# Kernel tuning notes

Hardware: AMD Instinct MI355X
Metric: run time of the kernel (lower is better)

The kernel has to match this reference:

```python
import jax, jax.numpy as jnp
import numpy as np

B, C, L = 16, 256, 2048

def setup_inputs() -> dict:
    key = jax.random.key(0)
    k1, k2, k3, k4 = jax.random.split(key, 4)
    return {
        "proj_query": jax.random.normal(k1, (B, C, L), dtype=jnp.float32),
        "proj_key": jax.random.normal(k2, (B, C, L), dtype=jnp.float32),
        "proj_val": jax.random.normal(k3, (B, C, L), dtype=jnp.float32),
        "padding_mask": jax.random.uniform(k4, (B, 1, L), dtype=jnp.float32),
    }

def reference(proj_query, proj_key, proj_val, padding_mask):
    c = proj_query.shape[1]
    # energy[b,l,m] = sum_c Q[b,c,l] * K[b,c,m]  -> (B, L, L)
    energy = jnp.einsum("bcl,bcm->blm", proj_query, proj_key) / jnp.sqrt(jnp.float32(c))
    # log-additive padding mask (the tril mask in the source is dead code, never applied)
    logits = energy + jnp.log(padding_mask + 1e-9)
    attention = jax.nn.softmax(logits, axis=-1)
    # post-softmax multiplicative mask
    attention = attention * padding_mask
    # out[b,c,l] = sum_m V[b,c,m] * attention[b,l,m]  -> (B, C, L)
    out = jnp.einsum("bcm,blm->bcl", proj_val, attention)
    return out
```

## Files before the change

kernel.cpp:

```cpp
#include <hip/hip_runtime.h>
#include <hip/hip_bf16.h>

#define B_ 16
#define C_ 256
#define L_ 2048
#define MT 32

typedef __attribute__((ext_vector_type(8))) short bf16x8;
typedef __attribute__((ext_vector_type(4))) float f32x4;

#define CEXP 0.09016844005556021f

__device__ __forceinline__ short f2bf_rne(float f) {
    union { float f; unsigned u; } x; x.f = f;
    unsigned r = x.u + 0x7fffu + ((x.u >> 16) & 1u);
    return (short)(r >> 16);
}

__device__ __forceinline__ void gld_lds16(const void* g, void* l) {
    __builtin_amdgcn_global_load_lds(
        (const __attribute__((address_space(1))) void*)g,
        (__attribute__((address_space(3))) void*)l, 16, 0, 0);
}

__global__ __launch_bounds__(256) void prepass_kernel(
        const float* __restrict__ Kin, const float* __restrict__ Vin,
        const float* __restrict__ mask,
        short* __restrict__ Kt, short* __restrict__ Vb) {
    const int bid = blockIdx.x;
    const int t = threadIdx.x;
    if (bid < 512) {
        __shared__ unsigned short tile[64 * 256];
        const int b  = bid >> 5;
        const int l0 = (bid & 31) * 64;
        #pragma unroll
        for (int iter = 0; iter < 16; ++iter) {
            int idx = iter * 256 + t;
            int ci = idx >> 4;
            int lc = (idx & 15) * 4;
            float4 v = *(const float4*)(Kin + ((size_t)(b * C_ + ci)) * L_ + l0 + lc);
            float vv[4] = {v.x, v.y, v.z, v.w};
            #pragma unroll
            for (int j = 0; j < 4; ++j) {
                int l = lc + j;
                tile[l * 256 + (((ci >> 3) ^ (l & 31)) << 3) + (ci & 7)] =
                    (unsigned short)f2bf_rne(vv[j]);
            }
        }
        __syncthreads();
        #pragma unroll
        for (int iter = 0; iter < 8; ++iter) {
            int li = iter * 8 + (t >> 5);
            int ck = t & 31;
            uint4 val = *(const uint4*)(tile + li * 256 + ((ck ^ (li & 31)) << 3));
            *(uint4*)(Kt + ((size_t)(b * L_ + l0 + li)) * C_ + ck * 8) = val;
        }
    } else {
        size_t e = ((size_t)(bid - 512) * 256 + t) * 8;
        int b = (int)(e >> 19);
        int m = (int)(e & (L_ - 1));
        const float4 v0 = *(const float4*)(Vin + e);
        const float4 v1 = *(const float4*)(Vin + e + 4);
        const float* mp = mask + ((size_t)b << 11) + m;
        const float4 m0 = *(const float4*)mp;
        const float4 m1 = *(const float4*)(mp + 4);
        uint4 o;
        o.x = (unsigned)(unsigned short)f2bf_rne(v0.x * m0.x)
            | ((unsigned)(unsigned short)f2bf_rne(v0.y * m0.y) << 16);
        o.y = (unsigned)(unsigned short)f2bf_rne(v0.z * m0.z)
            | ((unsigned)(unsigned short)f2bf_rne(v0.w * m0.w) << 16);
        o.z = (unsigned)(unsigned short)f2bf_rne(v1.x * m1.x)
            | ((unsigned)(unsigned short)f2bf_rne(v1.y * m1.y) << 16);
        o.w = (unsigned)(unsigned short)f2bf_rne(v1.z * m1.z)
            | ((unsigned)(unsigned short)f2bf_rne(v1.w * m1.w) << 16);
        *(uint4*)(Vb + e) = o;
    }
}

__device__ __forceinline__ void stage_K(const short* __restrict__ Ksrc,
                                        short* Ks, int m0, int t) {
    #pragma unroll
    for (int rr = 0; rr < 2; ++rr) {
        int G = rr * 512 + t;
        int m = G >> 5, p = G & 31;
        gld_lds16(Ksrc + ((size_t)(m0 + m) << 8) + ((p ^ m) << 3), Ks + G * 8);
    }
}

__device__ __forceinline__ void load_V(bf16x8 (&vf)[2], const short* __restrict__ Vw, int m0) {
    #pragma unroll
    for (int ct = 0; ct < 2; ++ct)
        vf[ct] = *(const bf16x8*)(Vw + (size_t)(ct * 16) * L_ + m0);
}

#define O_PHASE(PBUF, VF)                                                                  \
  {                                                                                        \
    _Pragma("unroll")                                                                      \
    for (int lt = 0; lt < 4; ++lt) {                                                       \
      bf16x8 af = *(const bf16x8*)((PBUF) + (16 * lt + 4 * (n & 3) + (n >> 2)) * 40 + 8 * q); \
      _Pragma("unroll")                                                                    \
      for (int ct = 0; ct < 2; ++ct)                                                       \
        Oacc[lt][ct] =                                                                     \
            __builtin_amdgcn_mfma_f32_16x16x32_bf16(af, (VF)[ct], Oacc[lt][ct], 0, 0, 0);  \
    }                                                                                      \
  }

#define S_PHASE(KS, PW0)                                                                   \
  {                                                                                        \
    f32x4 Sa = fzero, Sb = fzero;                                                          \
    const short* Krow = (KS) + (16 * mt + n) * 256;                                        \
    _Pragma("unroll")                                                                      \
    for (int ks = 0; ks < 4; ++ks) {                                                       \
      bf16x8 bfa = *(const bf16x8*)(Krow + (((4 * ks + q) ^ (16 * mt + n)) << 3));         \
      bf16x8 bfb = *(const bf16x8*)(Krow + (((4 * (ks + 4) + q) ^ (16 * mt + n)) << 3));   \
      Sa = __builtin_amdgcn_mfma_f32_16x16x32_bf16(qf[ks], bfa, Sa, 0, 0, 0);              \
      Sb = __builtin_amdgcn_mfma_f32_16x16x32_bf16(qf[ks + 4], bfb, Sb, 0, 0, 0);          \
    }                                                                                      \
    _Pragma("unroll")                                                                      \
    for (int r = 0; r < 4; ++r) {                                                          \
      float p0 = wv * exp2f(Sa[r] + Sb[r]);                                                \
      dn[r] += p0;                                                                         \
      (PW0)[(4 * r) * 40] = f2bf_rne(p0);                                                  \
    }                                                                                      \
  }

__global__ __launch_bounds__(512, 4) void attn_main(
        const float* __restrict__ Qin,
        const short* __restrict__ Kt,
        const short* __restrict__ Vb,
        const float* __restrict__ mask,
        float* __restrict__ out) {
    __shared__ __align__(16) char smem[43520];
    short* KsB0 = (short*)smem;
    short* KsB1 = (short*)(smem + 16384);
    short* PA   = (short*)(smem + 32768);
    short* PB   = (short*)(smem + 37888);
    float* Dsh  = (float*)(smem + 43008);

    const int t = threadIdx.x;
    const int w = t >> 6, lane = t & 63, q = lane >> 4, n = lane & 15;
    const int g = w & 3, mt = w >> 2;

    const int b  = blockIdx.x & 15;
    const int l0 = (blockIdx.x >> 4) * 64;

    const short* Ksrc = Kt + (size_t)b * (L_ * C_);
    const short* Vsrc = Vb + (size_t)b * (C_ * L_);
    const float* mrow = mask + (size_t)b * L_;
    const short* Vw   = Vsrc + (size_t)(32 * w + n) * L_ + 8 * q;
    short* Pw0A = PA + (16 * g + q) * 40 + 16 * mt + n;
    short* Pw0B = PB + (16 * g + q) * 40 + 16 * mt + n;

    bf16x8 qf[8];
    {
        const float* Qb = Qin + (size_t)b * (C_ * L_) + (l0 + 16 * g + n);
        #pragma unroll
        for (int ks = 0; ks < 8; ++ks) {
            bf16x8 v;
            #pragma unroll
            for (int j = 0; j < 8; ++j) {
                float f = Qb[(size_t)(32 * ks + 8 * q + j) * L_];
                v[j] = f2bf_rne(f * CEXP);
            }
            qf[ks] = v;
        }
    }

    const f32x4 fzero = {0.f, 0.f, 0.f, 0.f};
    f32x4 Oacc[4][2];
    #pragma unroll
    for (int i = 0; i < 4; ++i)
        #pragma unroll
        for (int j = 0; j < 2; ++j) Oacc[i][j] = fzero;
    float dn[4] = {0.f, 0.f, 0.f, 0.f};

    stage_K(Ksrc, KsB0, 0, t);
    bf16x8 vfA[2], vfB[2];
    load_V(vfA, Vw, 0);
    float wv = mrow[16 * mt + n] + 1e-9f;

    #pragma unroll 1
    for (int it2 = 0; it2 < L_ / MT / 2; ++it2) {
        const int m0a = it2 * (2 * MT);
        const int m0b = m0a + MT;

        __syncthreads();
        if (m0a != 0) O_PHASE(PB, vfB)
        stage_K(Ksrc, KsB1, m0a + MT, t);
        load_V(vfB, Vw, m0a + MT);
        float wvn0 = mrow[m0a + MT + 16 * mt + n] + 1e-9f;
        S_PHASE(KsB0, Pw0A)
        wv = wvn0;

        __syncthreads();
        O_PHASE(PA, vfA)
        float wvn1 = 0.f;
        if (m0b + MT < L_) {
            stage_K(Ksrc, KsB0, m0b + MT, t);
            load_V(vfA, Vw, m0b + MT);
            wvn1 = mrow[m0b + MT + 16 * mt + n] + 1e-9f;
        }
        S_PHASE(KsB1, Pw0B)
        wv = wvn1;
    }

    __syncthreads();
    O_PHASE(PB, vfB)

    #pragma unroll
    for (int d = 1; d < 16; d <<= 1) {
        #pragma unroll
        for (int r = 0; r < 4; ++r)
            dn[r] += __shfl_xor(dn[r], d, 64);
    }
    if (n == 0) {
        #pragma unroll
        for (int r = 0; r < 4; ++r)
            Dsh[mt * 64 + 16 * g + 4 * q + r] = dn[r];
    }
    __syncthreads();

    float rden[4][4];
    #pragma unroll
    for (int lt = 0; lt < 4; ++lt)
        #pragma unroll
        for (int r = 0; r < 4; ++r) {
            int l = 16 * lt + 4 * q + r;
            rden[lt][r] = 1.0f / (Dsh[l] + Dsh[64 + l]);
        }

    float* ob = out + (size_t)b * (C_ * L_) + l0;
    #pragma unroll
    for (int lt = 0; lt < 4; ++lt)
        #pragma unroll
        for (int ct = 0; ct < 2; ++ct) {
            int c = 32 * w + 16 * ct + n;
            float4 val;
            val.x = Oacc[lt][ct][0] * rden[lt][0];
            val.y = Oacc[lt][ct][1] * rden[lt][1];
            val.z = Oacc[lt][ct][2] * rden[lt][2];
            val.w = Oacc[lt][ct][3] * rden[lt][3];
            *(float4*)(ob + (size_t)c * L_ + 16 * lt + 4 * q) = val;
        }
}

extern "C" void kernel_launch(void* const* d_in, const int* in_sizes, int n_in,
                              void* d_out, int out_size, void* d_ws, size_t ws_size,
                              hipStream_t stream) {
    const float* Q    = (const float*)d_in[0];
    const float* K    = (const float*)d_in[1];
    const float* V    = (const float*)d_in[2];
    const float* mask = (const float*)d_in[3];
    float* out = (float*)d_out;

    short* Kt = (short*)d_ws;
    short* Vb = Kt + (size_t)B_ * L_ * C_;

    prepass_kernel<<<4608, 256, 0, stream>>>(K, V, mask, Kt, Vb);
    attn_main<<<512, 512, 0, stream>>>(Q, Kt, Vb, mask, out);
}
```

Measured before the change: 236.7 us.

## Restructure attention into per-wave 32x32 MFMA tiles with register-resident P

Replaces the 16x16x32 MFMA split, where waves shared S/P through LDS buffers, with a layout in which each wave owns 32 query rows across all 256 channels. It uses 32x32x16 MFMAs and keeps the probability tile in registers, feeding it straight into the PV MFMA. This removes the LDS round-trip and cross-wave dependency for P and reads V directly from global memory. The launch changes to 256 blocks of 256 threads at one block per CU. That raises register pressure and lowers occupancy, which risks poor latency hiding of the global V loads.

Measured after the change: 413.3 us. +74.6%, slower.

```diff
diff --git a/kernel.cpp b/kernel.cpp
--- a/kernel.cpp
+++ b/kernel.cpp
@@ -4,10 +4,13 @@
 #define B_ 16
 #define C_ 256
 #define L_ 2048
-#define MT 32
+#define KVB 32
+#define NT (L_ / KVB)
 
 typedef __attribute__((ext_vector_type(8))) short bf16x8;
-typedef __attribute__((ext_vector_type(4))) float f32x4;
+typedef __attribute__((ext_vector_type(4))) short bf16x4;
+typedef __attribute__((ext_vector_type(4))) unsigned u32x4;
+typedef __attribute__((ext_vector_type(16))) float f32x16;
 
 #define CEXP 0.09016844005556021f
 
@@ -80,167 +83,146 @@
 __device__ __forceinline__ void stage_K(const short* __restrict__ Ksrc,
                                         short* Ks, int m0, int t) {
     #pragma unroll
-    for (int rr = 0; rr < 2; ++rr) {
-        int G = rr * 512 + t;
+    for (int rr = 0; rr < 4; ++rr) {
+        int G = rr * 256 + t;
         int m = G >> 5, p = G & 31;
         gld_lds16(Ksrc + ((size_t)(m0 + m) << 8) + ((p ^ m) << 3), Ks + G * 8);
     }
 }
 
-__device__ __forceinline__ void load_V(bf16x8 (&vf)[2], const short* __restrict__ Vw, int m0) {
-    #pragma unroll
-    for (int ct = 0; ct < 2; ++ct)
-        vf[ct] = *(const bf16x8*)(Vw + (size_t)(ct * 16) * L_ + m0);
-}
-
-#define O_PHASE(PBUF, VF)                                                                  \
-  {                                                                                        \
-    _Pragma("unroll")                                                                      \
-    for (int lt = 0; lt < 4; ++lt) {                                                       \
-      bf16x8 af = *(const bf16x8*)((PBUF) + (16 * lt + 4 * (n & 3) + (n >> 2)) * 40 + 8 * q); \
-      _Pragma("unroll")                                                                    \
-      for (int ct = 0; ct < 2; ++ct)                                                       \
-        Oacc[lt][ct] =                                                                     \
-            __builtin_amdgcn_mfma_f32_16x16x32_bf16(af, (VF)[ct], Oacc[lt][ct], 0, 0, 0);  \
-    }                                                                                      \
+#define TILE_BODY(KS, M0)                                                                   \
+  {                                                                                         \
+    const short* Krow = (KS) + ln * 256;                                                    \
+    bf16x8 kf[16];                                                                          \
+    _Pragma("unroll")                                                                       \
+    for (int ki = 0; ki < 16; ++ki)                                                         \
+      kf[ki] = *(const bf16x8*)(Krow + (((2 * ki + h) ^ ln) << 3));                         \
+    bf16x4 vq[8][4];                                                                        \
+    _Pragma("unroll")                                                                       \
+    for (int ct = 0; ct < 8; ++ct)                                                          \
+      _Pragma("unroll")                                                                     \
+      for (int s = 0; s < 4; ++s)                                                           \
+        vq[ct][s] = *(const bf16x4*)(Vsrc + (size_t)(32 * ct + ln) * L_ + (M0) + 8 * s + 4 * h); \
+    float4 mk[4];                                                                           \
+    _Pragma("unroll")                                                                       \
+    for (int s = 0; s < 4; ++s) mk[s] = *(const float4*)(mrow + (M0) + 8 * s + 4 * h);      \
+    f32x16 s0 = z16, s1 = z16;                                                              \
+    _Pragma("unroll")                                                                       \
+    for (int ki = 0; ki < 8; ++ki)                                                          \
+      s0 = __builtin_amdgcn_mfma_f32_32x32x16_bf16(kf[ki], qf[ki], s0, 0, 0, 0);            \
+    _Pragma("unroll")                                                                       \
+    for (int ki = 8; ki < 16; ++ki)                                                         \
+      s1 = __builtin_amdgcn_mfma_f32_32x32x16_bf16(kf[ki], qf[ki], s1, 0, 0, 0);            \
+    unsigned pw[8];                                                                         \
+    _Pragma("unroll")                                                                       \
+    for (int r2 = 0; r2 < 8; ++r2) {                                                        \
+      const int ra = 2 * r2, rb = 2 * r2 + 1;                                               \
+      float fa = (mk[ra >> 2][ra & 3] + 1e-9f) * exp2f(s0[ra] + s1[ra]);                    \
+      float fb = (mk[rb >> 2][rb & 3] + 1e-9f) * exp2f(s0[rb] + s1[rb]);                    \
+      dn += fa + fb;                                                                        \
+      pw[r2] = (unsigned)(unsigned short)f2bf_rne(fa)                                       \
+             | ((unsigned)(unsigned short)f2bf_rne(fb) << 16);                              \
+    }                                                                                       \
+    u32x4 pa0u = {pw[0], pw[1], pw[2], pw[3]};                                              \
+    u32x4 pa1u = {pw[4], pw[5], pw[6], pw[7]};                                              \
+    bf16x8 pa0 = __builtin_bit_cast(bf16x8, pa0u);                                          \
+    bf16x8 pa1 = __builtin_bit_cast(bf16x8, pa1u);                                          \
+    _Pragma("unroll")                                                                       \
+    for (int ct = 0; ct < 8; ++ct) {                                                        \
+      bf16x8 v0 = __builtin_shufflevector(vq[ct][0], vq[ct][1], 0, 1, 2, 3, 4, 5, 6, 7);    \
+      bf16x8 v1 = __builtin_shufflevector(vq[ct][2], vq[ct][3], 0, 1, 2, 3, 4, 5, 6, 7);    \
+      Oacc[ct] = __builtin_amdgcn_mfma_f32_32x32x16_bf16(pa0, v0, Oacc[ct], 0, 0, 0);       \
+      Oacc[ct] = __builtin_amdgcn_mfma_f32_32x32x16_bf16(pa1, v1, Oacc[ct], 0, 0, 0);       \
+    }                                                                                       \
   }
 
-#define S_PHASE(KS, PW0)                                                                   \
-  {                                                                                        \
-    f32x4 Sa = fzero, Sb = fzero;                                                          \
-    const short* Krow = (KS) + (16 * mt + n) * 256;                                        \
-    _Pragma("unroll")                                                                      \
-    for (int ks = 0; ks < 4; ++ks) {                                                       \
-      bf16x8 bfa = *(const bf16x8*)(Krow + (((4 * ks + q) ^ (16 * mt + n)) << 3));         \
-      bf16x8 bfb = *(const bf16x8*)(Krow + (((4 * (ks + 4) + q) ^ (16 * mt + n)) << 3));   \
-      Sa = __builtin_amdgcn_mfma_f32_16x16x32_bf16(qf[ks], bfa, Sa, 0, 0, 0);              \
-      Sb = __builtin_amdgcn_mfma_f32_16x16x32_bf16(qf[ks + 4], bfb, Sb, 0, 0, 0);          \
-    }                                                                                      \
-    _Pragma("unroll")                                                                      \
-    for (int r = 0; r < 4; ++r) {                                                          \
-      float p0 = wv * exp2f(Sa[r] + Sb[r]);                                                \
-      dn[r] += p0;                                                                         \
-      (PW0)[(4 * r) * 40] = f2bf_rne(p0);                                                  \
-    }                                                                                      \
-  }
-
-__global__ __launch_bounds__(512, 4) void attn_main(
+__global__ __launch_bounds__(256, 1) void attn_main(
         const float* __restrict__ Qin,
         const short* __restrict__ Kt,
         const short* __restrict__ Vb,
         const float* __restrict__ mask,
         float* __restrict__ out) {
-    __shared__ __align__(16) char smem[43520];
+    __shared__ __align__(16) char smem[33280];
     short* KsB0 = (short*)smem;
     short* KsB1 = (short*)(smem + 16384);
-    short* PA   = (short*)(smem + 32768);
-    short* PB   = (short*)(smem + 37888);
-    float* Dsh  = (float*)(smem + 43008);
+    float* Dsh  = (float*)(smem + 32768);
 
     const int t = threadIdx.x;
-    const int w = t >> 6, lane = t & 63, q = lane >> 4, n = lane & 15;
-    const int g = w & 3, mt = w >> 2;
+    const int w = t >> 6, lane = t & 63;
+    const int ln = lane & 31, h = lane >> 5;
 
     const int b  = blockIdx.x & 15;
-    const int l0 = (blockIdx.x >> 4) * 64;
+    const int l0 = (blockIdx.x >> 4) * 128;
+    const int lw = l0 + 32 * w;
 
     const short* Ksrc = Kt + (size_t)b * (L_ * C_);
     const short* Vsrc = Vb + (size_t)b * (C_ * L_);
     const float* mrow = mask + (size_t)b * L_;
-    const short* Vw   = Vsrc + (size_t)(32 * w + n) * L_ + 8 * q;
-    short* Pw0A = PA + (16 * g + q) * 40 + 16 * mt + n;
-    short* Pw0B = PB + (16 * g + q) * 40 + 16 * mt + n;
-
-    bf16x8 qf[8];
+
+    stage_K(Ksrc, KsB0, 0, t);
+
+    bf16x8 qf[16];
     {
-        const float* Qb = Qin + (size_t)b * (C_ * L_) + (l0 + 16 * g + n);
-        #pragma unroll
-        for (int ks = 0; ks < 8; ++ks) {
+        const float* Qb = Qin + (size_t)b * (C_ * L_) + (lw + ln);
+        #pragma unroll
+        for (int ki = 0; ki < 16; ++ki) {
             bf16x8 v;
             #pragma unroll
             for (int j = 0; j < 8; ++j) {
-                float f = Qb[(size_t)(32 * ks + 8 * q + j) * L_];
+                float f = Qb[(size_t)(16 * ki + 8 * h + j) * L_];
                 v[j] = f2bf_rne(f * CEXP);
             }
-            qf[ks] = v;
-        }
-    }
-
-    const f32x4 fzero = {0.f, 0.f, 0.f, 0.f};
-    f32x4 Oacc[4][2];
-    #pragma unroll
-    for (int i = 0; i < 4; ++i)
-        #pragma unroll
-        for (int j = 0; j < 2; ++j) Oacc[i][j] = fzero;
-    float dn[4] = {0.f, 0.f, 0.f, 0.f};
-
-    stage_K(Ksrc, KsB0, 0, t);
-    bf16x8 vfA[2], vfB[2];
-    load_V(vfA, Vw, 0);
-    float wv = mrow[16 * mt + n] + 1e-9f;
+            qf[ki] = v;
+        }
+    }
+
+    const f32x16 z16 = {0.f,0.f,0.f,0.f,0.f,0.f,0.f,0.f,0.f,0.f,0.f,0.f,0.f,0.f,0.f,0.f};
+    f32x16 Oacc[8];
+    #pragma unroll
+    for (int ct = 0; ct < 8; ++ct) Oacc[ct] = z16;
+    float dn = 0.f;
+
+    __syncthreads();
 
     #pragma unroll 1
-    for (int it2 = 0; it2 < L_ / MT / 2; ++it2) {
-        const int m0a = it2 * (2 * MT);
-        const int m0b = m0a + MT;
-
+    for (int it2 = 0; it2 < NT / 2; ++it2) {
+        const int m0a = it2 * (2 * KVB);
+        const int m0b = m0a + KVB;
+
+        stage_K(Ksrc, KsB1, m0b, t);
+        TILE_BODY(KsB0, m0a)
         __syncthreads();
-        if (m0a != 0) O_PHASE(PB, vfB)
-        stage_K(Ksrc, KsB1, m0a + MT, t);
-        load_V(vfB, Vw, m0a + MT);
-        float wvn0 = mrow[m0a + MT + 16 * mt + n] + 1e-9f;
-        S_PHASE(KsB0, Pw0A)
-        wv = wvn0;
-
+
+        if (m0b + KVB < L_) stage_K(Ksrc, KsB0, m0b + KVB, t);
+        TILE_BODY(KsB1, m0b)
         __syncthreads();
-        O_PHASE(PA, vfA)
-        float wvn1 = 0.f;
-        if (m0b + MT < L_) {
-            stage_K(Ksrc, KsB0, m0b + MT, t);
-            load_V(vfA, Vw, m0b + MT);
-            wvn1 = mrow[m0b + MT + 16 * mt + n] + 1e-9f;
-        }
-        S_PHASE(KsB1, Pw0B)
-        wv = wvn1;
-    }
-
+    }
+
+    dn += __shfl_xor(dn, 32, 64);
+    if (h == 0) Dsh[32 * w + ln] = dn;
     __syncthreads();
-    O_PHASE(PB, vfB)
-
-    #pragma unroll
-    for (int d = 1; d < 16; d <<= 1) {
-        #pragma unroll
-        for (int r = 0; r < 4; ++r)
-            dn[r] += __shfl_xor(dn[r], d, 64);
-    }
-    if (n == 0) {
-        #pragma unroll
-        for (int r = 0; r < 4; ++r)
-            Dsh[mt * 64 + 16 * g + 4 * q + r] = dn[r];
-    }
-    __syncthreads();
-
-    float rden[4][4];
-    #pragma unroll
-    for (int lt = 0; lt < 4; ++lt)
-        #pragma unroll
-        for (int r = 0; r < 4; ++r) {
-            int l = 16 * lt + 4 * q + r;
-            rden[lt][r] = 1.0f / (Dsh[l] + Dsh[64 + l]);
-        }
-
-    float* ob = out + (size_t)b * (C_ * L_) + l0;
-    #pragma unroll
-    for (int lt = 0; lt < 4; ++lt)
-        #pragma unroll
-        for (int ct = 0; ct < 2; ++ct) {
-            int c = 32 * w + 16 * ct + n;
+
+    float4 rden[4];
+    #pragma unroll
+    for (int s = 0; s < 4; ++s) {
+        float4 dsv = *(const float4*)(Dsh + 32 * w + 8 * s + 4 * h);
+        rden[s].x = 1.0f / dsv.x;
+        rden[s].y = 1.0f / dsv.y;
+        rden[s].z = 1.0f / dsv.z;
+        rden[s].w = 1.0f / dsv.w;
+    }
+
+    float* ob = out + (size_t)b * (C_ * L_);
+    #pragma unroll
+    for (int ct = 0; ct < 8; ++ct)
+        #pragma unroll
+        for (int s = 0; s < 4; ++s) {
             float4 val;
-            val.x = Oacc[lt][ct][0] * rden[lt][0];
-            val.y = Oacc[lt][ct][1] * rden[lt][1];
-            val.z = Oacc[lt][ct][2] * rden[lt][2];
-            val.w = Oacc[lt][ct][3] * rden[lt][3];
-            *(float4*)(ob + (size_t)c * L_ + 16 * lt + 4 * q) = val;
+            val.x = Oacc[ct][4 * s + 0] * rden[s].x;
+            val.y = Oacc[ct][4 * s + 1] * rden[s].y;
+            val.z = Oacc[ct][4 * s + 2] * rden[s].z;
+            val.w = Oacc[ct][4 * s + 3] * rden[s].w;
+            *(float4*)(ob + (size_t)(32 * ct + ln) * L_ + lw + 8 * s + 4 * h) = val;
         }
 }
 
@@ -257,5 +239,5 @@
     short* Vb = Kt + (size_t)B_ * L_ * C_;
 
     prepass_kernel<<<4608, 256, 0, stream>>>(K, V, mask, Kt, Vb);
-    attn_main<<<512, 512, 0, stream>>>(Q, Kt, Vb, mask, out);
-}
+    attn_main<<<256, 256, 0, stream>>>(Q, Kt, Vb, mask, out);
+}
```
